# Performance work log

Measured on AMD Instinct MI355X. Metric: run time of the kernel, lower is better.

## Reference

```python
import jax, jax.numpy as jnp
import numpy as np

B, S, E = 2, 4096, 2560
H, HKV, D = 8, 4, 256
WINDOW = 1024
SOFTCAP = 50.0
SCALING = 256.0 ** -0.5  # query_pre_attn_scalar = 256
EPS = 1e-6
MASK_VAL = -2.3819763e38


def rms_norm(x, w):
    # RMSNorm with add_unit_offset=True, computed in float32
    xf = x.astype(jnp.float32)
    out = xf * jax.lax.rsqrt(jnp.mean(xf * xf, axis=-1, keepdims=True) + EPS)
    return (out * (1.0 + w.astype(jnp.float32))).astype(x.dtype)


def apply_rotary_emb(x, cos, sin):
    # x: [B, S, h, D]; cos/sin: [S, D/2]; half-split rotation
    x1, x2 = jnp.split(x, 2, axis=-1)
    c = cos[None, :, None, :]
    s = sin[None, :, None, :]
    return jnp.concatenate([x1 * c - x2 * s, x2 * c + x1 * s], axis=-1)


def setup_inputs() -> dict:
    key = jax.random.key(0)
    ks = jax.random.split(key, 6)
    hidden_states = jax.random.normal(ks[0], (B, S, E), dtype=jnp.float32)
    # RoPE frequencies, theta=10000
    inv_freq = 1.0 / (10000.0 ** (np.arange(0, D, 2, dtype=np.float32) / D))
    t = np.arange(S, dtype=np.float32)
    freqs = np.outer(t, inv_freq)  # [S, D/2]
    freqs_cos = jnp.asarray(np.cos(freqs), dtype=jnp.float32)
    freqs_sin = jnp.asarray(np.sin(freqs), dtype=jnp.float32)
    kv_write_indices = jnp.arange(S, dtype=jnp.int32)
    k_cache = jnp.zeros((B, S, HKV, D), dtype=jnp.float32)
    v_cache = jnp.zeros((B, S, HKV, D), dtype=jnp.float32)
    # causal mask and causal+sliding-window mask (additive)
    i = np.arange(S)[:, None]
    j = np.arange(S)[None, :]
    causal = j <= i
    sliding = causal & ((i - j) < WINDOW)
    mask = jnp.asarray(np.where(causal, 0.0, MASK_VAL), dtype=jnp.float32)
    mask = jnp.broadcast_to(mask[None, None], (B, 1, S, S))
    local_mask = jnp.asarray(np.where(sliding, 0.0, MASK_VAL), dtype=jnp.float32)
    local_mask = jnp.broadcast_to(local_mask[None, None], (B, 1, S, S))
    w_qkv = jax.random.normal(ks[1], ((H + 2 * HKV) * D, E), dtype=jnp.float32) * (E ** -0.5)
    w_o = jax.random.normal(ks[2], (E, H * D), dtype=jnp.float32) * ((H * D) ** -0.5)
    q_norm_w = jnp.zeros((D,), dtype=jnp.float32)
    k_norm_w = jnp.zeros((D,), dtype=jnp.float32)
    return dict(hidden_states=hidden_states, freqs_cos=freqs_cos, freqs_sin=freqs_sin,
                kv_write_indices=kv_write_indices, k_cache=k_cache, v_cache=v_cache,
                mask=mask, local_mask=local_mask, w_qkv=w_qkv, w_o=w_o,
                q_norm_w=q_norm_w, k_norm_w=k_norm_w)


def reference(hidden_states, freqs_cos, freqs_sin, kv_write_indices, k_cache, v_cache,
              mask, local_mask, w_qkv, w_o, q_norm_w, k_norm_w):
    bsz, input_len, _ = hidden_states.shape
    qkv = jnp.einsum('bse,fe->bsf', hidden_states, w_qkv)
    xq, xk, xv = jnp.split(qkv, [H * D, H * D + HKV * D], axis=-1)
    xq = xq.reshape(bsz, input_len, H, D)
    xk = xk.reshape(bsz, input_len, HKV, D)
    xv = xv.reshape(bsz, input_len, HKV, D)
    # QK RMSNorm
    xq = rms_norm(xq, q_norm_w)
    xk = rms_norm(xk, k_norm_w)
    # RoPE
    xq = apply_rotary_emb(xq, freqs_cos, freqs_sin)
    xk = apply_rotary_emb(xk, freqs_cos, freqs_sin)
    # KV cache write
    k_cache = k_cache.at[:, kv_write_indices].set(xk)
    v_cache = v_cache.at[:, kv_write_indices].set(xv)
    kv_len = k_cache.shape[1]
    # GQA expand: [B, T, HKV, D] -> [B, T, H, D]
    nrep = H // HKV
    key = jnp.repeat(k_cache, nrep, axis=2)
    value = jnp.repeat(v_cache, nrep, axis=2)
    q = jnp.transpose(xq, (0, 2, 1, 3)) * SCALING   # [B, H, S, D]
    k = jnp.transpose(key, (0, 2, 1, 3))            # [B, H, T, D]
    v = jnp.transpose(value, (0, 2, 1, 3))
    scores = jnp.einsum('bhqd,bhkd->bhqk', q, k)
    # logit softcapping
    scores = jnp.tanh(scores / SOFTCAP) * SOFTCAP
    # attn_type == LOCAL_SLIDING -> use local (sliding-window) mask
    scores = scores + local_mask
    probs = jax.nn.softmax(scores.astype(jnp.float32), axis=-1).astype(q.dtype)
    out = jnp.einsum('bhqk,bhkd->bhqd', probs, v)
    out = jnp.transpose(out, (0, 2, 1, 3)).reshape(bsz, input_len, H * D)
    return jnp.einsum('bsf,ef->bse', out, w_o)
```

## Files before the change

### kernel.cpp

```cpp
#include <hip/hip_runtime.h>
#include <stdint.h>
#include <stddef.h>

#define B_    2
#define S_    4096
#define E_    2560
#define H_    8
#define HKV_  4
#define D_    256
#define F_    4096
#define HD_   2048
#define WIN_  1024

typedef __bf16 bf16;
typedef bf16  bf16x8 __attribute__((ext_vector_type(8)));
typedef bf16  bf16x4 __attribute__((ext_vector_type(4)));
typedef float f32x4  __attribute__((ext_vector_type(4)));
typedef uint32_t u32;

__device__ __forceinline__ void gl_lds16(const void* g, void* l) {
  __builtin_amdgcn_global_load_lds((const __attribute__((address_space(1))) void*)g,
                                   (__attribute__((address_space(3))) void*)l, 16, 0, 0);
}

__device__ __forceinline__ void bar_mf() {
  asm volatile("" ::: "memory");
  __builtin_amdgcn_s_barrier();
  asm volatile("" ::: "memory");
}

__device__ __forceinline__ u32 pkbf16(float a, float b) {
  union { bf16 h[2]; u32 u; } cv;
  cv.h[0] = (bf16)a; cv.h[1] = (bf16)b; return cv.u;
}

__global__ __launch_bounds__(256) void to_bf16_plain(const float* __restrict__ src,
                                                     bf16* __restrict__ dst, int n) {
  const int i = (blockIdx.x * 256 + threadIdx.x) * 8;
  if (i >= n) return;
  f32x4 a = *(const f32x4*)(src + i);
  f32x4 b = *(const f32x4*)(src + i + 4);
  bf16x8 o;
#pragma unroll
  for (int j = 0; j < 4; ++j) { o[j] = (bf16)a[j]; o[j + 4] = (bf16)b[j]; }
  *(bf16x8*)(dst + i) = o;
}

template <int EPI, int BN>
__global__ __launch_bounds__(512, 2) void gemm_8ph(
    const bf16* __restrict__ A, const bf16* __restrict__ Bw, int Kd, int NT,
    bf16* __restrict__ qo, bf16* __restrict__ ko, bf16* __restrict__ vto,
    float* __restrict__ C, int Nout, int row_base) {
  constexpr int NBH = BN / 128;
  constexpr int JT  = BN / 64;
  __shared__ bf16 Lds[2][2 + NBH][128 * 64];

  const int tid  = threadIdx.x;
  const int lane = tid & 63;
  const int wave = tid >> 6;
  const int wm   = wave >> 2;
  const int wn   = wave & 3;
  const int l16  = lane & 15;
  const int quad = lane >> 4;

  const int nwg  = gridDim.x * gridDim.y;
  const int obid = blockIdx.y * gridDim.x + blockIdx.x;
  const int bid  = (obid & 7) * (nwg >> 3) + (obid >> 3);
  const int mt   = bid / gridDim.x;
  const int ntl  = bid - mt * gridDim.x;
  const int row0 = mt * 256, col0 = ntl * BN;

  const bf16* Ah[2] = {A + (size_t)row0 * Kd, A + (size_t)(row0 + 128) * Kd};
  const bf16* Bh[2] = {Bw + (size_t)col0 * Kd,
                       Bw + (size_t)(col0 + (NBH == 2 ? 128 : 0)) * Kd};

  auto stage = [&](int dbf, int hf, const bf16* src, int k0) {
#pragma unroll
    for (int i = 0; i < 2; ++i) {
      const int g = tid + i * 512;
      const int r = g >> 3, c = g & 7;
      gl_lds16(src + (size_t)r * Kd + k0 + ((c ^ (r & 7)) << 3),
               &Lds[dbf][hf][0] + g * 8);
    }
  };
  auto rdA = [&](int dbf, int i, int ks) -> bf16x8 {
    const int r = i * 16 + l16;
    return *(const bf16x8*)&Lds[dbf][wm][r * 64 + (((ks * 4 + quad) ^ (r & 7)) << 3)];
  };
  auto rdB = [&](int dbf, int j, int ks) -> bf16x8 {
    const int colt = wn * (BN / 4) + j * 16 + l16;
    const int r = colt & 127;
    return *(const bf16x8*)&Lds[dbf][2 + (colt >> 7)][r * 64 + (((ks * 4 + quad) ^ (r & 7)) << 3)];
  };

  f32x4 acc[8][JT] = {};

  stage(0, 0, Ah[0], 0); stage(0, 1, Ah[1], 0);
#pragma unroll
  for (int h = 0; h < NBH; ++h) stage(0, 2 + h, Bh[h], 0);
  if (NT > 1) {
#pragma unroll
    for (int h = 0; h < NBH; ++h) stage(1, 2 + h, Bh[h], 64);
  }
  if constexpr (NBH == 2) asm volatile("s_waitcnt vmcnt(4)" ::: "memory");
  else                    asm volatile("s_waitcnt vmcnt(2)" ::: "memory");
  bar_mf();

  int db = 0;
  for (int t = 0; t < NT; ++t, db ^= 1) {
    const int k1 = (t + 1) * 64, k2 = (t + 2) * 64;
    const bool st1 = (t + 1 < NT), st2 = (t + 2 < NT);

    bf16x8 bfr[JT][2], a01[2][2], a23[2][2], a45[2][2], a67[2][2];
#pragma unroll
    for (int j = 0; j < JT; ++j) { bfr[j][0] = rdB(db, j, 0); bfr[j][1] = rdB(db, j, 1); }
#pragma unroll
    for (int i = 0; i < 2; ++i) { a01[i][0] = rdA(db, i, 0);     a01[i][1] = rdA(db, i, 1); }
#pragma unroll
    for (int i = 0; i < 2; ++i) { a23[i][0] = rdA(db, i + 2, 0); a23[i][1] = rdA(db, i + 2, 1); }
    if (st1) { stage(db ^ 1, 0, Ah[0], k1); stage(db ^ 1, 1, Ah[1], k1); }

    __builtin_amdgcn_s_setprio(1);
#pragma unroll
    for (int i = 0; i < 2; ++i)
#pragma unroll
      for (int j = 0; j < JT; ++j) {
        acc[i][j] = __builtin_amdgcn_mfma_f32_16x16x32_bf16(a01[i][0], bfr[j][0], acc[i][j], 0, 0, 0);
        acc[i][j] = __builtin_amdgcn_mfma_f32_16x16x32_bf16(a01[i][1], bfr[j][1], acc[i][j], 0, 0, 0);
      }
    __builtin_amdgcn_s_setprio(0);

#pragma unroll
    for (int i = 0; i < 2; ++i) { a45[i][0] = rdA(db, i + 4, 0); a45[i][1] = rdA(db, i + 4, 1); }

    __builtin_amdgcn_s_setprio(1);
#pragma unroll
    for (int i = 0; i < 2; ++i)
#pragma unroll
      for (int j = 0; j < JT; ++j) {
        acc[i + 2][j] = __builtin_amdgcn_mfma_f32_16x16x32_bf16(a23[i][0], bfr[j][0], acc[i + 2][j], 0, 0, 0);
        acc[i + 2][j] = __builtin_amdgcn_mfma_f32_16x16x32_bf16(a23[i][1], bfr[j][1], acc[i + 2][j], 0, 0, 0);
      }
    __builtin_amdgcn_s_setprio(0);

    bar_mf();
    if (st2) {
      stage(db, 2, Bh[0], k2);
      if constexpr (NBH == 2) stage(db, 3, Bh[1], k2);
    }
#pragma unroll
    for (int i = 0; i < 2; ++i) { a67[i][0] = rdA(db, i + 6, 0); a67[i][1] = rdA(db, i + 6, 1); }

    __builtin_amdgcn_s_setprio(1);
#pragma unroll
    for (int i = 0; i < 2; ++i)
#pragma unroll
      for (int j = 0; j < JT; ++j) {
        acc[i + 4][j] = __builtin_amdgcn_mfma_f32_16x16x32_bf16(a45[i][0], bfr[j][0], acc[i + 4][j], 0, 0, 0);
        acc[i + 4][j] = __builtin_amdgcn_mfma_f32_16x16x32_bf16(a45[i][1], bfr[j][1], acc[i + 4][j], 0, 0, 0);
      }
    __builtin_amdgcn_s_setprio(0);

    __builtin_amdgcn_s_setprio(1);
#pragma unroll
    for (int i = 0; i < 2; ++i)
#pragma unroll
      for (int j = 0; j < JT; ++j) {
        acc[i + 6][j] = __builtin_amdgcn_mfma_f32_16x16x32_bf16(a67[i][0], bfr[j][0], acc[i + 6][j], 0, 0, 0);
        acc[i + 6][j] = __builtin_amdgcn_mfma_f32_16x16x32_bf16(a67[i][1], bfr[j][1], acc[i + 6][j], 0, 0, 0);
      }
    __builtin_amdgcn_s_setprio(0);

    if (st2) {
      if constexpr (NBH == 2) asm volatile("s_waitcnt vmcnt(4)" ::: "memory");
      else                    asm volatile("s_waitcnt vmcnt(2)" ::: "memory");
    } else {
      asm volatile("s_waitcnt vmcnt(0)" ::: "memory");
    }
    bar_mf();
  }

#pragma unroll
  for (int i = 0; i < 8; ++i) {
    const int rbase = row_base + row0 + wm * 128 + i * 16 + quad * 4;
#pragma unroll
    for (int j = 0; j < JT; ++j) {
      const int c = col0 + wn * (BN / 4) + j * 16 + l16;
      if constexpr (EPI == 1) {
        int head = c >> 8;
        const int d = c & 255;
        if (head < 12) {
          bf16* base; int nh;
          if (head < 8) { base = qo; nh = H_; }
          else          { base = ko; nh = HKV_; head -= 8; }
#pragma unroll
          for (int rr = 0; rr < 4; ++rr) {
            const int row = rbase + rr;
            const int bb = row >> 12, s = row & 4095;
            base[(((size_t)(bb * nh + head) * S_) + s) * D_ + d] = (bf16)acc[i][j][rr];
          }
        } else {
          const int kh = head - 12;
          const int bb = rbase >> 12, s0 = rbase & 4095;
          bf16x4 pk;
#pragma unroll
          for (int rr = 0; rr < 4; ++rr) pk[rr] = (bf16)acc[i][j][rr];
          *(bf16x4*)(vto + (((size_t)(bb * HKV_ + kh) * D_ + d) * S_ + s0)) = pk;
        }
      } else {
#pragma unroll
        for (int rr = 0; rr < 4; ++rr)
          C[(size_t)(rbase + rr) * Nout + c] = acc[i][j][rr];
      }
    }
  }
}

__global__ __launch_bounds__(192) void normrope2(
    bf16* __restrict__ q, bf16* __restrict__ k,
    const float* __restrict__ fcos, const float* __restrict__ fsin,
    const int* __restrict__ widx,
    const float* __restrict__ qnw, const float* __restrict__ knw) {
  const int bx  = blockIdx.x;
  const int b   = bx >> 12;
  const int s   = bx & 4095;
  const int tid = threadIdx.x;
  const int hh  = tid >> 4;
  const int g   = tid & 15;
  const int d0  = g * 16;

  const bool isq = (hh < 8);
  bf16* rowp = isq ? (q + (((size_t)(b * H_ + hh) * S_ + s) * D_ + d0))
                   : (k + (((size_t)(b * HKV_ + (hh - 8)) * S_ + s) * D_ + d0));
  float x[16];
  {
    bf16x8 v0 = *(const bf16x8*)rowp;
    bf16x8 v1 = *(const bf16x8*)(rowp + 8);
#pragma unroll
    for (int i = 0; i < 8; ++i) { x[i] = (float)v0[i]; x[i + 8] = (float)v1[i]; }
  }

  float ssq = 0.f;
#pragma unroll
  for (int i = 0; i < 16; ++i) ssq += x[i] * x[i];
#pragma unroll
  for (int off = 1; off < 16; off <<= 1) ssq += __shfl_xor(ssq, off);
  const float sc = rsqrtf(ssq * (1.0f / 256.0f) + 1e-6f);
  const float* w = isq ? qnw : knw;
#pragma unroll
  for (int i = 0; i < 16; ++i) x[i] = x[i] * sc * (1.0f + w[d0 + i]);

  const int fbase = (g < 8) ? d0 : (d0 - 128);
  const float* cp = fcos + (size_t)s * 128 + fbase;
  const float* sp = fsin + (size_t)s * 128 + fbase;
#pragma unroll
  for (int i = 0; i < 16; ++i) {
    const float c = cp[i], sn = sp[i];
    const float other = __shfl_xor(x[i], 8);
    x[i] = (g < 8) ? (x[i] * c - other * sn)
                   : (x[i] * c + other * sn);
  }
  if (isq) {
#pragma unroll
    for (int i = 0; i < 16; ++i) x[i] *= 0.0625f;
  }

  bf16x8 o0, o1;
#pragma unroll
  for (int i = 0; i < 8; ++i) { o0[i] = (bf16)x[i]; o1[i] = (bf16)x[i + 8]; }

  bf16* dstp = isq ? rowp
                   : (k + (((size_t)(b * HKV_ + (hh - 8)) * S_ + widx[s]) * D_ + d0));
  *(bf16x8*)dstp = o0;
  *(bf16x8*)(dstp + 8) = o1;
}

__global__ __launch_bounds__(256) void attn_mfma(const bf16* __restrict__ Q,
                                                 const bf16* __restrict__ K,
                                                 const bf16* __restrict__ Vt,
                                                 bf16* __restrict__ out) {
  __shared__ bf16 Ks[2][32 * 256];
  __shared__ bf16 Vs[2][256 * 32];

  const int hw  = blockIdx.x;
  const int lid = (hw & 7) * 128 + (hw >> 3);
  const int bx  = lid & 63;
  const int bh  = lid >> 6;
  const int b   = bh >> 3, h = bh & 7, kh = h >> 1;

  const int lane = threadIdx.x & 63;
  const int wave = threadIdx.x >> 6;
  const int l16  = lane & 15;
  const int qd   = lane >> 4;
  const int swz  = l16 & 7;

  const int q0w = bx * 64 + wave * 16;
  const int iq  = q0w + l16;

  const bf16* Kb = K  + ((size_t)(b * HKV_ + kh) * S_) * D_;
  const bf16* Vb = Vt + ((size_t)(b * HKV_ + kh) * D_) * S_;

  bf16x8 qf[8];
  {
    const bf16* qp = Q + (((size_t)(b * H_ + h) * S_ + iq) * D_) + qd * 8;
#pragma unroll
    for (int kc = 0; kc < 8; ++kc) qf[kc] = *(const bf16x8*)(qp + kc * 32);
  }

  f32x4 Od[16] = {};
  float lsum = 0.f;

  int lo = bx * 64 - (WIN_ - 1); if (lo < 0) lo = 0;
  lo &= ~31;
  const int t1 = bx * 64 + 32;

  auto stage = [&](int buf, int kt) {
#pragma unroll
    for (int i = 0; i < 4; ++i) {
      const int r0  = wave * 8 + i * 2;
      const int row = r0 + (lane >> 5);
      const int c   = lane & 31;
      const int pk = (((row >> 2) & 3) << 3) + ((row >> 4) << 2) + (row & 3);
      gl_lds16(Kb + (size_t)(kt + pk) * D_ + ((c ^ (row & 7)) * 8),
               &Ks[buf][r0 * 256] + lane * 8);
    }
#pragma unroll
    for (int i = 0; i < 4; ++i) {
      const int d0 = (wave * 4 + i) * 16;
      const int d  = d0 + (lane >> 2);
      gl_lds16(Vb + (size_t)d * S_ + kt + (lane & 3) * 8,
               &Vs[buf][d0 * 32] + lane * 8);
    }
  };

  stage(0, lo);
  int buf = 0;

  const float c1 = 0.05770780163555853f;
  const float c2 = -144.26950408889634f;

  for (int kt = lo; kt <= t1; kt += 32) {
    const bool pre = (kt + 32 <= t1);
    if (pre) {
      stage(buf ^ 1, kt + 32);
      asm volatile("s_waitcnt vmcnt(8)" ::: "memory");
    } else {
      asm volatile("s_waitcnt vmcnt(0)" ::: "memory");
    }
    __builtin_amdgcn_s_barrier();
    asm volatile("" ::: "memory");

    const bool dead = (kt > q0w + 15) || (kt + 31 < q0w - (WIN_ - 1));
    if (!dead) {
      f32x4 sacc[2] = {};
#pragma unroll
      for (int kc = 0; kc < 8; ++kc) {
        const int ch = ((kc * 4 + qd) ^ swz) * 8;
        bf16x8 k0 = *(const bf16x8*)&Ks[buf][l16 * 256 + ch];
        bf16x8 k1 = *(const bf16x8*)&Ks[buf][(l16 + 16) * 256 + ch];
        sacc[0] = __builtin_amdgcn_mfma_f32_16x16x32_bf16(k0, qf[kc], sacc[0], 0, 0, 0);
        sacc[1] = __builtin_amdgcn_mfma_f32_16x16x32_bf16(k1, qf[kc], sacc[1], 0, 0, 0);
      }

      const bool interior = (kt + 31 <= q0w) && (kt >= q0w - 1008);
      const int  kb0 = kt + qd * 8;
      float p[8];
#pragma unroll
      for (int t = 0; t < 2; ++t)
#pragma unroll
        for (int r = 0; r < 4; ++r) {
          const float x = sacc[t][r];
          const float wv = __builtin_amdgcn_rcpf(exp2f(x * c1) + 1.0f);
          float pp = exp2f(c2 * wv);
          if (!interior) {
            const int key = kb0 + t * 4 + r;
            pp = (key <= iq && (iq - key) < WIN_) ? pp : 0.f;
          }
          p[t * 4 + r] = pp;
          lsum += pp;
        }

      union { u32 u[4]; bf16x8 v; } pf;
      pf.u[0] = pkbf16(p[0], p[1]);
      pf.u[1] = pkbf16(p[2], p[3]);
      pf.u[2] = pkbf16(p[4], p[5]);
      pf.u[3] = pkbf16(p[6], p[7]);

#pragma unroll
      for (int dt = 0; dt < 16; ++dt) {
        bf16x8 vf = *(const bf16x8*)&Vs[buf][(dt * 16 + l16) * 32 + qd * 8];
        Od[dt] = __builtin_amdgcn_mfma_f32_16x16x32_bf16(vf, pf.v, Od[dt], 0, 0, 0);
      }
    }

    asm volatile("" ::: "memory");
    __builtin_amdgcn_s_barrier();
    buf ^= 1;
  }

  float l = lsum + __shfl_xor(lsum, 16);
  l += __shfl_xor(l, 32);
  const float inv = 1.f / l;
  bf16* op = out + ((size_t)b * S_ + iq) * HD_ + h * D_ + qd * 4;
#pragma unroll
  for (int dt = 0; dt < 16; ++dt) {
    bf16x4 o4;
#pragma unroll
    for (int r = 0; r < 4; ++r) o4[r] = (bf16)(Od[dt][r] * inv);
    *(bf16x4*)(op + dt * 16) = o4;
  }
}

extern "C" void kernel_launch(void* const* d_in, const int* in_sizes, int n_in,
                              void* d_out, int out_size, void* d_ws, size_t ws_size,
                              hipStream_t stream) {
  const float* hidden = (const float*)d_in[0];
  const float* fcos   = (const float*)d_in[1];
  const float* fsin   = (const float*)d_in[2];
  const int*   widx   = (const int*)d_in[3];
  const float* wqkv   = (const float*)d_in[8];
  const float* wo     = (const float*)d_in[9];
  const float* qnw    = (const float*)d_in[10];
  const float* knw    = (const float*)d_in[11];
  float* out = (float*)d_out;

  char* ws = (char*)d_ws;
  const size_t MB = 1024 * 1024;
  const bool big = ws_size >= 126 * MB;

  bf16* wb_bf = (bf16*)(ws);
  bf16* hb_bf = (bf16*)(ws + 20 * MB);
  bf16* q_ws  = (bf16*)(ws + (big ? 60 : 32) * MB);
  bf16* k_ws  = (bf16*)(ws + (big ? 92 : 64) * MB);
  bf16* vt_ws = (bf16*)(ws + (big ? 108 : 80) * MB);
  bf16* att_o = (bf16*)(ws);
  bf16* wo_bf = (bf16*)(ws + 32 * MB);

  to_bf16_plain<<<(F_ * E_ / 8 + 255) / 256, 256, 0, stream>>>(wqkv, wb_bf, F_ * E_);

  const int nch   = big ? 1 : 4;
  const int chrow = (B_ * S_) / nch;
  for (int c = 0; c < nch; ++c) {
    const int row_base = c * chrow;
    to_bf16_plain<<<(chrow * E_ / 8 + 255) / 256, 256, 0, stream>>>(
        hidden + (size_t)row_base * E_, hb_bf, chrow * E_);
    if (big)
      gemm_8ph<1, 256><<<dim3(F_ / 256, chrow / 256), 512, 0, stream>>>(
          hb_bf, wb_bf, E_, E_ / 64, q_ws, k_ws, vt_ws, nullptr, 0, row_base);
    else
      gemm_8ph<1, 128><<<dim3(F_ / 128, chrow / 256), 512, 0, stream>>>(
          hb_bf, wb_bf, E_, E_ / 64, q_ws, k_ws, vt_ws, nullptr, 0, row_base);
  }

  normrope2<<<dim3(B_ * S_), 192, 0, stream>>>(q_ws, k_ws, fcos, fsin, widx, qnw, knw);
  attn_mfma<<<dim3(1024), 256, 0, stream>>>(q_ws, k_ws, vt_ws, att_o);
  to_bf16_plain<<<(E_ * HD_ / 8 + 255) / 256, 256, 0, stream>>>(wo, wo_bf, E_ * HD_);
  gemm_8ph<0, 128><<<dim3(E_ / 128, (B_ * S_) / 256), 512, 0, stream>>>(
      att_o, wo_bf, HD_, HD_ / 64, nullptr, nullptr, nullptr, out, E_, 0);
  (void)in_sizes; (void)n_in; (void)out_size;
}
```

Before: 797.3 us.

## Double query rows per attention wave and swizzle V tile in LDS

Each attention wave now handles two 16-row query groups (128 queries per block, 512 blocks), so every K and V fragment read from LDS feeds two MFMAs. This halves LDS traffic and staging per query. It also XOR-swizzles the V tile layout to cut LDS bank conflicts, and uses the 256-wide tile for the output projection GEMM when `big` is set. In exchange, accumulator register pressure doubles (launch_bounds 256,2), causal tiles do more masked work, and there are fewer blocks to spread across the GPU.

```diff
diff --git a/kernel.cpp b/kernel.cpp
--- a/kernel.cpp
+++ b/kernel.cpp
@@ -275,17 +275,17 @@
   *(bf16x8*)(dstp + 8) = o1;
 }
 
-__global__ __launch_bounds__(256) void attn_mfma(const bf16* __restrict__ Q,
-                                                 const bf16* __restrict__ K,
-                                                 const bf16* __restrict__ Vt,
-                                                 bf16* __restrict__ out) {
+__global__ __launch_bounds__(256, 2) void attn_mfma(const bf16* __restrict__ Q,
+                                                    const bf16* __restrict__ K,
+                                                    const bf16* __restrict__ Vt,
+                                                    bf16* __restrict__ out) {
   __shared__ bf16 Ks[2][32 * 256];
   __shared__ bf16 Vs[2][256 * 32];
 
   const int hw  = blockIdx.x;
-  const int lid = (hw & 7) * 128 + (hw >> 3);
-  const int bx  = lid & 63;
-  const int bh  = lid >> 6;
+  const int lid = (hw & 7) * 64 + (hw >> 3);
+  const int bx  = lid & 31;
+  const int bh  = lid >> 5;
   const int b   = bh >> 3, h = bh & 7, kh = h >> 1;
 
   const int lane = threadIdx.x & 63;
@@ -294,25 +294,25 @@
   const int qd   = lane >> 4;
   const int swz  = l16 & 7;
 
-  const int q0w = bx * 64 + wave * 16;
-  const int iq  = q0w + l16;
+  const int q0w = bx * 128 + wave * 32;
 
   const bf16* Kb = K  + ((size_t)(b * HKV_ + kh) * S_) * D_;
   const bf16* Vb = Vt + ((size_t)(b * HKV_ + kh) * D_) * S_;
 
-  bf16x8 qf[8];
-  {
-    const bf16* qp = Q + (((size_t)(b * H_ + h) * S_ + iq) * D_) + qd * 8;
-#pragma unroll
-    for (int kc = 0; kc < 8; ++kc) qf[kc] = *(const bf16x8*)(qp + kc * 32);
-  }
-
-  f32x4 Od[16] = {};
-  float lsum = 0.f;
-
-  int lo = bx * 64 - (WIN_ - 1); if (lo < 0) lo = 0;
+  bf16x8 qf[2][8];
+#pragma unroll
+  for (int g = 0; g < 2; ++g) {
+    const bf16* qp = Q + (((size_t)(b * H_ + h) * S_ + q0w + g * 16 + l16) * D_) + qd * 8;
+#pragma unroll
+    for (int kc = 0; kc < 8; ++kc) qf[g][kc] = *(const bf16x8*)(qp + kc * 32);
+  }
+
+  f32x4 Od[2][16] = {};
+  float lsum[2] = {0.f, 0.f};
+
+  int lo = bx * 128 - (WIN_ - 1); if (lo < 0) lo = 0;
   lo &= ~31;
-  const int t1 = bx * 64 + 32;
+  const int t1 = bx * 128 + 96;
 
   auto stage = [&](int buf, int kt) {
 #pragma unroll
@@ -328,7 +328,8 @@
     for (int i = 0; i < 4; ++i) {
       const int d0 = (wave * 4 + i) * 16;
       const int d  = d0 + (lane >> 2);
-      gl_lds16(Vb + (size_t)d * S_ + kt + (lane & 3) * 8,
+      const int cs = (lane & 3) ^ ((lane >> 3) & 3);
+      gl_lds16(Vb + (size_t)d * S_ + kt + cs * 8,
                &Vs[buf][d0 * 32] + lane * 8);
     }
   };
@@ -350,46 +351,54 @@
     __builtin_amdgcn_s_barrier();
     asm volatile("" ::: "memory");
 
-    const bool dead = (kt > q0w + 15) || (kt + 31 < q0w - (WIN_ - 1));
+    const bool dead = (kt > q0w + 31) || (kt + 31 < q0w - (WIN_ - 1));
     if (!dead) {
-      f32x4 sacc[2] = {};
+      f32x4 sacc[2][2] = {};
 #pragma unroll
       for (int kc = 0; kc < 8; ++kc) {
         const int ch = ((kc * 4 + qd) ^ swz) * 8;
         bf16x8 k0 = *(const bf16x8*)&Ks[buf][l16 * 256 + ch];
         bf16x8 k1 = *(const bf16x8*)&Ks[buf][(l16 + 16) * 256 + ch];
-        sacc[0] = __builtin_amdgcn_mfma_f32_16x16x32_bf16(k0, qf[kc], sacc[0], 0, 0, 0);
-        sacc[1] = __builtin_amdgcn_mfma_f32_16x16x32_bf16(k1, qf[kc], sacc[1], 0, 0, 0);
-      }
-
-      const bool interior = (kt + 31 <= q0w) && (kt >= q0w - 1008);
-      const int  kb0 = kt + qd * 8;
-      float p[8];
-#pragma unroll
-      for (int t = 0; t < 2; ++t)
-#pragma unroll
-        for (int r = 0; r < 4; ++r) {
-          const float x = sacc[t][r];
-          const float wv = __builtin_amdgcn_rcpf(exp2f(x * c1) + 1.0f);
-          float pp = exp2f(c2 * wv);
-          if (!interior) {
-            const int key = kb0 + t * 4 + r;
-            pp = (key <= iq && (iq - key) < WIN_) ? pp : 0.f;
+        sacc[0][0] = __builtin_amdgcn_mfma_f32_16x16x32_bf16(k0, qf[0][kc], sacc[0][0], 0, 0, 0);
+        sacc[0][1] = __builtin_amdgcn_mfma_f32_16x16x32_bf16(k1, qf[0][kc], sacc[0][1], 0, 0, 0);
+        sacc[1][0] = __builtin_amdgcn_mfma_f32_16x16x32_bf16(k0, qf[1][kc], sacc[1][0], 0, 0, 0);
+        sacc[1][1] = __builtin_amdgcn_mfma_f32_16x16x32_bf16(k1, qf[1][kc], sacc[1][1], 0, 0, 0);
+      }
+
+      union { u32 u[4]; bf16x8 v; } pf[2];
+      const int kb0 = kt + qd * 8;
+#pragma unroll
+      for (int g = 0; g < 2; ++g) {
+        const int qg = q0w + g * 16;
+        const int iq = qg + l16;
+        const bool interior = (kt + 31 <= qg) && (kt >= qg - 1008);
+        float p[8];
+#pragma unroll
+        for (int t = 0; t < 2; ++t)
+#pragma unroll
+          for (int r = 0; r < 4; ++r) {
+            const float x = sacc[g][t][r];
+            const float wv = __builtin_amdgcn_rcpf(exp2f(x * c1) + 1.0f);
+            float pp = exp2f(c2 * wv);
+            if (!interior) {
+              const int key = kb0 + t * 4 + r;
+              pp = (key <= iq && (iq - key) < WIN_) ? pp : 0.f;
+            }
+            p[t * 4 + r] = pp;
+            lsum[g] += pp;
           }
-          p[t * 4 + r] = pp;
-          lsum += pp;
-        }
-
-      union { u32 u[4]; bf16x8 v; } pf;
-      pf.u[0] = pkbf16(p[0], p[1]);
-      pf.u[1] = pkbf16(p[2], p[3]);
-      pf.u[2] = pkbf16(p[4], p[5]);
-      pf.u[3] = pkbf16(p[6], p[7]);
+        pf[g].u[0] = pkbf16(p[0], p[1]);
+        pf[g].u[1] = pkbf16(p[2], p[3]);
+        pf[g].u[2] = pkbf16(p[4], p[5]);
+        pf[g].u[3] = pkbf16(p[6], p[7]);
+      }
 
 #pragma unroll
       for (int dt = 0; dt < 16; ++dt) {
-        bf16x8 vf = *(const bf16x8*)&Vs[buf][(dt * 16 + l16) * 32 + qd * 8];
-        Od[dt] = __builtin_amdgcn_mfma_f32_16x16x32_bf16(vf, pf.v, Od[dt], 0, 0, 0);
+        const int ch = (qd ^ ((l16 >> 1) & 3)) * 8;
+        bf16x8 vf = *(const bf16x8*)&Vs[buf][(dt * 16 + l16) * 32 + ch];
+        Od[0][dt] = __builtin_amdgcn_mfma_f32_16x16x32_bf16(vf, pf[0].v, Od[0][dt], 0, 0, 0);
+        Od[1][dt] = __builtin_amdgcn_mfma_f32_16x16x32_bf16(vf, pf[1].v, Od[1][dt], 0, 0, 0);
       }
     }
 
@@ -398,16 +407,20 @@
     buf ^= 1;
   }
 
-  float l = lsum + __shfl_xor(lsum, 16);
-  l += __shfl_xor(l, 32);
-  const float inv = 1.f / l;
-  bf16* op = out + ((size_t)b * S_ + iq) * HD_ + h * D_ + qd * 4;
-#pragma unroll
-  for (int dt = 0; dt < 16; ++dt) {
-    bf16x4 o4;
-#pragma unroll
-    for (int r = 0; r < 4; ++r) o4[r] = (bf16)(Od[dt][r] * inv);
-    *(bf16x4*)(op + dt * 16) = o4;
+#pragma unroll
+  for (int g = 0; g < 2; ++g) {
+    float l = lsum[g] + __shfl_xor(lsum[g], 16);
+    l += __shfl_xor(l, 32);
+    const float inv = 1.f / l;
+    const int iq = q0w + g * 16 + l16;
+    bf16* op = out + ((size_t)b * S_ + iq) * HD_ + h * D_ + qd * 4;
+#pragma unroll
+    for (int dt = 0; dt < 16; ++dt) {
+      bf16x4 o4;
+#pragma unroll
+      for (int r = 0; r < 4; ++r) o4[r] = (bf16)(Od[g][dt][r] * inv);
+      *(bf16x4*)(op + dt * 16) = o4;
+    }
   }
 }
 
@@ -453,9 +466,13 @@
   }
 
   normrope2<<<dim3(B_ * S_), 192, 0, stream>>>(q_ws, k_ws, fcos, fsin, widx, qnw, knw);
-  attn_mfma<<<dim3(1024), 256, 0, stream>>>(q_ws, k_ws, vt_ws, att_o);
+  attn_mfma<<<dim3(512), 256, 0, stream>>>(q_ws, k_ws, vt_ws, att_o);
   to_bf16_plain<<<(E_ * HD_ / 8 + 255) / 256, 256, 0, stream>>>(wo, wo_bf, E_ * HD_);
-  gemm_8ph<0, 128><<<dim3(E_ / 128, (B_ * S_) / 256), 512, 0, stream>>>(
-      att_o, wo_bf, HD_, HD_ / 64, nullptr, nullptr, nullptr, out, E_, 0);
+  if (big)
+    gemm_8ph<0, 256><<<dim3(E_ / 256, (B_ * S_) / 256), 512, 0, stream>>>(
+        att_o, wo_bf, HD_, HD_ / 64, nullptr, nullptr, nullptr, out, E_, 0);
+  else
+    gemm_8ph<0, 128><<<dim3(E_ / 128, (B_ * S_) / 256), 512, 0, stream>>>(
+        att_o, wo_bf, HD_, HD_ / 64, nullptr, nullptr, nullptr, out, E_, 0);
   (void)in_sizes; (void)n_in; (void)out_size;
 }
```

After: 800.4 us. About the same (+0.4%).
